# Performance work log

Measured on AMD Instinct MI355X. Metric: run time of the kernel, lower is better.

## Reference

```python
import jax, jax.numpy as jnp
import numpy as np

# PennyLane default.gaussian conventions: hbar = 2, means vector in (x, p) per-wire
# quadratures; expval(X(w)) = mu_x[w], expval(P(w)) = mu_p[w].
_SQRT_2HBAR = 2.0  # sqrt(2 * hbar) with hbar = 2


def _run_circuit(x, disp, sq, bs):
    """Evolve Gaussian means for all samples at once.

    x: [B, N] input displacements (phi=0)
    disp, sq: [L, N, 2] (magnitude, phase)
    bs: [L, N-1, 2] (theta-logit, phi)
    Returns (mu_x, mu_p) each [B, N].
    """
    L, N = disp.shape[0], disp.shape[1]
    mx = _SQRT_2HBAR * x          # initial Displacement(x_i, 0) on each wire
    mp = jnp.zeros_like(x)
    for l in range(L):
        # Displacement(a, phi) on every wire (different wires commute)
        a, dphi = disp[l, :, 0], disp[l, :, 1]
        mx = mx + _SQRT_2HBAR * a * jnp.cos(dphi)
        mp = mp + _SQRT_2HBAR * a * jnp.sin(dphi)
        # Squeezing(|r|, phi) symplectic [[ch-cp*sh, -sp*sh], [-sp*sh, ch+cp*sh]]
        r, sphi = jnp.abs(sq[l, :, 0]), sq[l, :, 1]
        ch, sh = jnp.cosh(r), jnp.sinh(r)
        cp, sp = jnp.cos(sphi), jnp.sin(sphi)
        mx, mp = (ch - cp * sh) * mx - sp * sh * mp, -sp * sh * mx + (ch + cp * sh) * mp
        # Beamsplitter(sigmoid(t), phi) on (w, w+1): sequential, overlapping wires
        for w in range(N - 1):
            th = jax.nn.sigmoid(bs[l, w, 0])
            bphi = bs[l, w, 1]
            ct, st = jnp.cos(th), jnp.sin(th)
            cpb, spb = jnp.cos(bphi), jnp.sin(bphi)
            x1, x2 = mx[:, w], mx[:, w + 1]
            p1, p2 = mp[:, w], mp[:, w + 1]
            nx1 = ct * x1 - cpb * st * x2 - spb * st * p2
            nx2 = cpb * st * x1 + ct * x2 - spb * st * p1
            np1 = spb * st * x2 + ct * p1 - cpb * st * p2
            np2 = spb * st * x1 + cpb * st * p1 + ct * p2
            mx = mx.at[:, w].set(nx1).at[:, w + 1].set(nx2)
            mp = mp.at[:, w].set(np1).at[:, w + 1].set(np2)
    return mx, mp


def setup_inputs() -> dict:
    key = jax.random.key(0)
    k1, k2, k3, k4 = jax.random.split(key, 4)
    B, N, L = 1048576, 16, 6
    return {
        "x": jax.random.normal(k1, (B, N), dtype=jnp.float32),
        "displacements": jax.random.normal(k2, (2, L, N, 2), dtype=jnp.float32),
        "squeezing": jax.random.normal(k3, (2, L, N, 2), dtype=jnp.float32),
        "beamsplitter": jax.random.normal(k4, (2, L, N - 1, 2), dtype=jnp.float32),
    }


def reference(x, displacements, squeezing, beamsplitter):
    # Parameter set 0 feeds the X-quadrature circuit, set 1 the P-quadrature circuit.
    mx0, _ = _run_circuit(x, displacements[0], squeezing[0], beamsplitter[0])
    _, mp1 = _run_circuit(x, displacements[1], squeezing[1], beamsplitter[1])
    return jnp.concatenate([mx0, mp1], axis=-1)  # [B, 2N]
```

## Files before the change

kernel.cpp:

```cpp
#include <hip/hip_runtime.h>
#include <math.h>

#define NM 16
#define NL 6
#define NW 15
#define S2H 2.0f
#define TILES 4

typedef float v4f __attribute__((ext_vector_type(4)));
typedef short bf16x8 __attribute__((ext_vector_type(8)));
typedef float f32x16 __attribute__((ext_vector_type(16)));


__device__ __forceinline__ unsigned short f2bf(float f) {
    union { float f; unsigned int u; } v; v.f = f;
    unsigned int r = (v.u + 0x7fffu + ((v.u >> 16) & 1u)) >> 16;
    return (unsigned short)r;
}

__global__ __launch_bounds__(640) void cv_precompute(
    const float* __restrict__ disp,
    const float* __restrict__ sq,
    const float* __restrict__ bs,
    float* __restrict__ ws)
{
    __shared__ float dxc[2][NL][NM], dpc[2][NL][NM];
    __shared__ float s00[2][NL][NM], s01[2][NL][NM], s11[2][NL][NM];
    __shared__ float bct[2][NL][NW], bcs[2][NL][NW], bss[2][NL][NW];

    int t = threadIdx.x;
    if (t < 192) {
        int c = t / 96, rem = t % 96, l = rem / NM, n = rem % NM;
        float a  = disp[((c*NL + l)*NM + n)*2 + 0];
        float ph = disp[((c*NL + l)*NM + n)*2 + 1];
        dxc[c][l][n] = S2H * a * cosf(ph);
        dpc[c][l][n] = S2H * a * sinf(ph);
    } else if (t < 384) {
        int i = t - 192;
        int c = i / 96, rem = i % 96, l = rem / NM, n = rem % NM;
        float r  = fabsf(sq[((c*NL + l)*NM + n)*2 + 0]);
        float ph = sq[((c*NL + l)*NM + n)*2 + 1];
        float ch = coshf(r), sh = sinhf(r);
        float cp = cosf(ph), sp = sinf(ph);
        s00[c][l][n] = ch - cp*sh;
        s01[c][l][n] = -sp*sh;
        s11[c][l][n] = ch + cp*sh;
    } else if (t < 564) {
        int i = t - 384;
        int c = i / 90, rem = i % 90, l = rem / NW, w = rem % NW;
        float z  = bs[((c*NL + l)*NW + w)*2 + 0];
        float ph = bs[((c*NL + l)*NW + w)*2 + 1];
        float th = 1.0f / (1.0f + expf(-z));
        float ct = cosf(th), st = sinf(th);
        bct[c][l][w] = ct;
        bcs[c][l][w] = cosf(ph) * st;
        bss[c][l][w] = sinf(ph) * st;
    }
    __syncthreads();

    if (t >= 34) return;
    int c = t / 17;
    int col = t % 17;
    bool isBias = (col == NM);

    float mx[NM], mp[NM];
    #pragma unroll
    for (int n = 0; n < NM; ++n) { mx[n] = 0.f; mp[n] = 0.f; }
    if (!isBias) mx[col] = S2H;

    for (int l = 0; l < NL; ++l) {
        if (isBias) {
            #pragma unroll
            for (int n = 0; n < NM; ++n) { mx[n] += dxc[c][l][n]; mp[n] += dpc[c][l][n]; }
        }
        #pragma unroll
        for (int n = 0; n < NM; ++n) {
            float a = s00[c][l][n], b = s01[c][l][n], d = s11[c][l][n];
            float nx  = a*mx[n] + b*mp[n];
            float npp = b*mx[n] + d*mp[n];
            mx[n] = nx; mp[n] = npp;
        }
        #pragma unroll
        for (int w = 0; w < NW; ++w) {
            float ct = bct[c][l][w], cst = bcs[c][l][w], sst = bss[c][l][w];
            float x1 = mx[w], x2 = mx[w+1], p1 = mp[w], p2 = mp[w+1];
            mx[w]   = ct*x1  - cst*x2 - sst*p2;
            mx[w+1] = cst*x1 + ct*x2  - sst*p1;
            mp[w]   = sst*x2 + ct*p1  - cst*p2;
            mp[w+1] = sst*x1 + cst*p1 + ct*p2;
        }
    }

    ushort* bfp  = (ushort*)ws;
    float* biasp = ws + 256;
    if (!isBias) {
        #pragma unroll
        for (int n = 0; n < NM; ++n) {
            int row = 16*c + n;
            float val = (c == 0) ? mx[n] : mp[n];
            int lane = row + 32 * (col >> 3);
            int slot = col & 7;
            bfp[lane * 8 + slot] = f2bf(val);
        }
    } else {
        #pragma unroll
        for (int n = 0; n < NM; ++n)
            biasp[16*c + n] = (c == 0) ? mx[n] : mp[n];
    }
}

__global__ __launch_bounds__(256, 4) void cv_apply(
    const float* __restrict__ x,
    const float* __restrict__ ws,
    float* __restrict__ out,
    long long B)
{
    __shared__ float st[128 * 32];
    const int t = threadIdx.x;
    const int lane = t & 63;
    const int wave = t >> 6;
    const int n = lane & 31;
    const int kg = lane >> 5;

    const bf16x8 bfrag = *(const bf16x8*)((const ushort*)ws + lane * 8);
    const float  bn    = (ws + 256)[n];

    const long long base = (long long)blockIdx.x * (128 * TILES);

    float4 va[TILES][2];
    #pragma unroll
    for (int tt = 0; tt < TILES; ++tt) {
        const long long row = base + tt * 128 + wave * 32 + n;
        if (row < B) {
            const float4* xp = (const float4*)(x + row * 16 + kg * 8);
            va[tt][0] = xp[0];
            va[tt][1] = xp[1];
        } else {
            va[tt][0] = make_float4(0.f, 0.f, 0.f, 0.f);
            va[tt][1] = make_float4(0.f, 0.f, 0.f, 0.f);
        }
    }

    f32x16 acc[TILES];
    #pragma unroll
    for (int tt = 0; tt < TILES; ++tt) {
        bf16x8 af;
        af[0] = (short)f2bf(va[tt][0].x); af[1] = (short)f2bf(va[tt][0].y);
        af[2] = (short)f2bf(va[tt][0].z); af[3] = (short)f2bf(va[tt][0].w);
        af[4] = (short)f2bf(va[tt][1].x); af[5] = (short)f2bf(va[tt][1].y);
        af[6] = (short)f2bf(va[tt][1].z); af[7] = (short)f2bf(va[tt][1].w);
        f32x16 cin;
        #pragma unroll
        for (int r = 0; r < 16; ++r) cin[r] = bn;
        acc[tt] = __builtin_amdgcn_mfma_f32_32x32x16_bf16(af, bfrag, cin, 0, 0, 0);
    }

    #pragma unroll
    for (int tt = 0; tt < TILES; ++tt) {
        if (tt) __syncthreads();
        #pragma unroll
        for (int r = 0; r < 16; ++r) {
            int m = (r & 3) + 8 * (r >> 2) + 4 * kg;
            st[(wave * 32 + m) * 32 + n] = acc[tt][r];
        }
        __syncthreads();

        const long long tb = base + tt * 128;
        v4f* __restrict__ op = (v4f*)(out + tb * 32);
        long long rem = B - tb;
        if (rem <= 0) continue;
        const long long u4max = (rem < 128 ? rem : 128) * 8;
        const float4* stv = (const float4*)st;
        #pragma unroll
        for (int i = 0; i < 4; ++i) {
            int u = i * 256 + t;
            if (u < u4max) {
                float4 v = stv[u];
                v4f r; r[0]=v.x; r[1]=v.y; r[2]=v.z; r[3]=v.w;
                __builtin_nontemporal_store(r, op + u);
            }
        }
    }
}

extern "C" void kernel_launch(void* const* d_in, const int* in_sizes, int n_in,
                              void* d_out, int out_size, void* d_ws, size_t ws_size,
                              hipStream_t stream) {
    const float* x    = (const float*)d_in[0];
    const float* disp = (const float*)d_in[1];
    const float* sq   = (const float*)d_in[2];
    const float* bs   = (const float*)d_in[3];
    float* ws  = (float*)d_ws;
    float* out = (float*)d_out;

    long long B = in_sizes[0] / NM;

    cv_precompute<<<1, 640, 0, stream>>>(disp, sq, bs, ws);

    int blocks = (int)((B + 128 * TILES - 1) / (128 * TILES));
    cv_apply<<<blocks, 256, 0, stream>>>(x, ws, out, B);
}
```

Measured before the change: 44.01 us.

## Swap MFMA operand order so outputs store directly without LDS transpose

The weight fragment now goes in the A operand and the input in the B operand, so each lane's accumulator holds output features of one sample. Results are written straight to global memory as float4 stores, which removes the shared-memory staging buffer and the block barriers. The bias is loaded per accumulator row, and each wave now owns a contiguous chunk of samples. The tradeoff is that global stores become strided 16-byte writes per lane instead of fully coalesced nontemporal stores, and the occupancy hint drops from 4 to 3.

```diff
diff --git a/kernel.cpp b/kernel.cpp
--- a/kernel.cpp
+++ b/kernel.cpp
@@ -109,30 +109,34 @@
     }
 }
 
-__global__ __launch_bounds__(256, 4) void cv_apply(
+__global__ __launch_bounds__(256, 3) void cv_apply(
     const float* __restrict__ x,
     const float* __restrict__ ws,
     float* __restrict__ out,
     long long B)
 {
-    __shared__ float st[128 * 32];
     const int t = threadIdx.x;
     const int lane = t & 63;
     const int wave = t >> 6;
-    const int n = lane & 31;
+    const int s32 = lane & 31;
     const int kg = lane >> 5;
 
-    const bf16x8 bfrag = *(const bf16x8*)((const ushort*)ws + lane * 8);
-    const float  bn    = (ws + 256)[n];
+    const bf16x8 wfrag = *(const bf16x8*)((const ushort*)ws + lane * 8);
 
-    const long long base = (long long)blockIdx.x * (128 * TILES);
+    const float* biasp = ws + 256;
+    float bias16[16];
+    #pragma unroll
+    for (int r = 0; r < 16; ++r)
+        bias16[r] = biasp[(r & 3) + 8 * (r >> 2) + 4 * kg];
+
+    const long long wbase = ((long long)blockIdx.x * 4 + wave) * (32 * TILES);
 
     float4 va[TILES][2];
     #pragma unroll
     for (int tt = 0; tt < TILES; ++tt) {
-        const long long row = base + tt * 128 + wave * 32 + n;
-        if (row < B) {
-            const float4* xp = (const float4*)(x + row * 16 + kg * 8);
+        const long long smp = wbase + tt * 32 + s32;
+        if (smp < B) {
+            const float4* xp = (const float4*)(x + smp * 16 + kg * 8);
             va[tt][0] = xp[0];
             va[tt][1] = xp[1];
         } else {
@@ -141,43 +145,28 @@
         }
     }
 
-    f32x16 acc[TILES];
     #pragma unroll
     for (int tt = 0; tt < TILES; ++tt) {
-        bf16x8 af;
-        af[0] = (short)f2bf(va[tt][0].x); af[1] = (short)f2bf(va[tt][0].y);
-        af[2] = (short)f2bf(va[tt][0].z); af[3] = (short)f2bf(va[tt][0].w);
-        af[4] = (short)f2bf(va[tt][1].x); af[5] = (short)f2bf(va[tt][1].y);
-        af[6] = (short)f2bf(va[tt][1].z); af[7] = (short)f2bf(va[tt][1].w);
+        bf16x8 xf;
+        xf[0] = (short)f2bf(va[tt][0].x); xf[1] = (short)f2bf(va[tt][0].y);
+        xf[2] = (short)f2bf(va[tt][0].z); xf[3] = (short)f2bf(va[tt][0].w);
+        xf[4] = (short)f2bf(va[tt][1].x); xf[5] = (short)f2bf(va[tt][1].y);
+        xf[6] = (short)f2bf(va[tt][1].z); xf[7] = (short)f2bf(va[tt][1].w);
+
         f32x16 cin;
         #pragma unroll
-        for (int r = 0; r < 16; ++r) cin[r] = bn;
-        acc[tt] = __builtin_amdgcn_mfma_f32_32x32x16_bf16(af, bfrag, cin, 0, 0, 0);
-    }
+        for (int r = 0; r < 16; ++r) cin[r] = bias16[r];
 
-    #pragma unroll
-    for (int tt = 0; tt < TILES; ++tt) {
-        if (tt) __syncthreads();
-        #pragma unroll
-        for (int r = 0; r < 16; ++r) {
-            int m = (r & 3) + 8 * (r >> 2) + 4 * kg;
-            st[(wave * 32 + m) * 32 + n] = acc[tt][r];
-        }
-        __syncthreads();
+        f32x16 acc = __builtin_amdgcn_mfma_f32_32x32x16_bf16(wfrag, xf, cin, 0, 0, 0);
 
-        const long long tb = base + tt * 128;
-        v4f* __restrict__ op = (v4f*)(out + tb * 32);
-        long long rem = B - tb;
-        if (rem <= 0) continue;
-        const long long u4max = (rem < 128 ? rem : 128) * 8;
-        const float4* stv = (const float4*)st;
-        #pragma unroll
-        for (int i = 0; i < 4; ++i) {
-            int u = i * 256 + t;
-            if (u < u4max) {
-                float4 v = stv[u];
-                v4f r; r[0]=v.x; r[1]=v.y; r[2]=v.z; r[3]=v.w;
-                __builtin_nontemporal_store(r, op + u);
+        const long long smp = wbase + tt * 32 + s32;
+        if (smp < B) {
+            float* op = out + smp * 32 + 4 * kg;
+            #pragma unroll
+            for (int g = 0; g < 4; ++g) {
+                v4f r4; r4[0] = acc[g*4+0]; r4[1] = acc[g*4+1];
+                r4[2] = acc[g*4+2]; r4[3] = acc[g*4+3];
+                *(v4f*)(op + g * 8) = r4;
             }
         }
     }
@@ -197,6 +186,7 @@
 
     cv_precompute<<<1, 640, 0, stream>>>(disp, sq, bs, ws);
 
-    int blocks = (int)((B + 128 * TILES - 1) / (128 * TILES));
+    long long per_block = 4LL * 32 * TILES;
+    int blocks = (int)((B + per_block - 1) / per_block);
     cv_apply<<<blocks, 256, 0, stream>>>(x, ws, out, B);
 }
```

New measurement: 47.69 us. 8.3% more time.
